# Optimization experiments

Hardware: AMD Instinct MI355X
Metric: run time of the kernel (lower is better)

## Reference

```python
import jax, jax.numpy as jnp
import numpy as np

B, K, D_H = 4096, 64, 512
N_AGENTS = 64  # sigma value == N_AGENTS means 'unassigned'
NEG_INF = -1e9


def setup_inputs() -> dict:
    key = jax.random.key(0)
    k1, k2, k3 = jax.random.split(key, 3)
    h = jax.random.normal(k1, (B, K, D_H), dtype=jnp.float32)
    # per-agent attention keys (init std=0.01 as in the torch module)
    keys = jax.random.normal(k2, (N_AGENTS, D_H), dtype=jnp.float32) * 0.01
    sigma = jax.random.randint(k3, (B, K), 0, N_AGENTS + 1)  # N_AGENTS == unassigned
    return {"h": h, "keys": keys, "sigma": sigma}


def reference(h, keys, sigma):
    # h: (B, K, d_h); keys: (n_agents, d_h); sigma: (B, K) int ids
    n_agents = keys.shape[0]
    valid = sigma < n_agents                      # (B, K) mask; id==n_agents -> unassigned
    idx = jnp.where(valid, sigma, 0)              # safe gather index
    w = keys[idx]                                 # (B, K, d_h) gathered agent keys
    logits = jnp.einsum('bkd,bkd->bk', w, h)      # per-slot dot-product score
    logits = jnp.where(valid, logits, NEG_INF)
    alpha = jax.nn.softmax(logits, axis=1)        # softmax over K slots
    return jnp.einsum('bk,bkd->bd', alpha, h)     # (B, d_h) weighted pooling
```

## Files before the change

### kernel.cpp

```cpp
#include <hip/hip_runtime.h>


constexpr int K  = 64;
constexpr int D  = 512;
constexpr int NA = 64;
#define NEG_INF (-1e9f)

__global__ __launch_bounds__(512)
void bda_kernel(const float* __restrict__ h, const float* __restrict__ keys,
                const int* __restrict__ sigma, float* __restrict__ out) {
    const int b    = blockIdx.x;
    const int tid  = threadIdx.x;
    const int w    = tid >> 6;
    const int lane = tid & 63;

    __shared__ float lg[K];
    __shared__ __align__(16) float obuf[8 * D];

    const float* hb = h + (size_t)b * (K * D);
    float4 h0[8], h1[8];

#pragma unroll
    for (int kk = 0; kk < 8; ++kk) {
        const int k = (w << 3) + kk;
        const float* hrow = hb + k * D + (lane << 3);
        h0[kk] = ((const float4*)hrow)[0];
        h1[kk] = ((const float4*)hrow)[1];

        const int sg = sigma[b * K + k];
        float dacc = NEG_INF;
        if (sg < NA) {
            const float* krow = keys + sg * D + (lane << 3);
            const float4 k0 = ((const float4*)krow)[0];
            const float4 k1 = ((const float4*)krow)[1];
            dacc = h0[kk].x * k0.x + h0[kk].y * k0.y
                 + h0[kk].z * k0.z + h0[kk].w * k0.w
                 + h1[kk].x * k1.x + h1[kk].y * k1.y
                 + h1[kk].z * k1.z + h1[kk].w * k1.w;
#pragma unroll
            for (int off = 32; off > 0; off >>= 1)
                dacc += __shfl_xor(dacc, off, 64);
        }
        if (lane == 0) lg[k] = dacc;
    }
    __syncthreads();

    const float v = lg[lane];
    float m = v;
#pragma unroll
    for (int off = 32; off > 0; off >>= 1)
        m = fmaxf(m, __shfl_xor(m, off, 64));
    float s = __expf(v - m);
#pragma unroll
    for (int off = 32; off > 0; off >>= 1)
        s += __shfl_xor(s, off, 64);
    const float inv_s = 1.0f / s;

    float4 a0 = make_float4(0.f, 0.f, 0.f, 0.f);
    float4 a1 = make_float4(0.f, 0.f, 0.f, 0.f);
#pragma unroll
    for (int kk = 0; kk < 8; ++kk) {
        const int k = (w << 3) + kk;
        const float al = __expf(lg[k] - m) * inv_s;
        a0.x += al * h0[kk].x;  a0.y += al * h0[kk].y;
        a0.z += al * h0[kk].z;  a0.w += al * h0[kk].w;
        a1.x += al * h1[kk].x;  a1.y += al * h1[kk].y;
        a1.z += al * h1[kk].z;  a1.w += al * h1[kk].w;
    }
    float* ob = obuf + w * D + (lane << 3);
    ((float4*)ob)[0] = a0;
    ((float4*)ob)[1] = a1;
    __syncthreads();

    float r = 0.f;
#pragma unroll
    for (int w2 = 0; w2 < 8; ++w2)
        r += obuf[w2 * D + tid];
    out[(size_t)b * D + tid] = r;
}

extern "C" void kernel_launch(void* const* d_in, const int* in_sizes, int n_in,
                              void* d_out, int out_size, void* d_ws, size_t ws_size,
                              hipStream_t stream) {
    const float* h     = (const float*)d_in[0];
    const float* keys  = (const float*)d_in[1];
    const int*   sigma = (const int*)d_in[2];
    float*       out   = (float*)d_out;
    const int B = in_sizes[2] / K;
    bda_kernel<<<dim3(B), dim3(512), 0, stream>>>(h, keys, sigma, out);
}
```

Baseline: 671.4 us.

## Hoist all h loads, vectorize sigma loads, and use transposed butterfly reduction

Issues all 16 float4 loads of h up front, before any reduction, so the memory requests overlap instead of being serialized behind the per-row shuffle reductions. Sigma is now read as two int4 vector loads, and keys are loaded unconditionally with a clamped index so there is no divergent branch. The eight per-row 64-lane reductions are merged into a transposed butterfly that needs fewer shuffles in total. Launch bounds now request 4 blocks per CU, which caps registers and may cause spills given the 64 floats of h held per thread.

```diff
diff --git a/kernel.cpp b/kernel.cpp
--- a/kernel.cpp
+++ b/kernel.cpp
@@ -6,7 +6,7 @@
 constexpr int NA = 64;
 #define NEG_INF (-1e9f)
 
-__global__ __launch_bounds__(512)
+__global__ __launch_bounds__(512, 4)
 void bda_kernel(const float* __restrict__ h, const float* __restrict__ keys,
                 const int* __restrict__ sigma, float* __restrict__ out) {
     const int b    = blockIdx.x;
@@ -18,39 +18,61 @@
     __shared__ __align__(16) float obuf[8 * D];
 
     const float* hb = h + (size_t)b * (K * D);
+
     float4 h0[8], h1[8];
+#pragma unroll
+    for (int kk = 0; kk < 8; ++kk) {
+        const float* hrow = hb + ((w << 3) + kk) * D + (lane << 3);
+        h0[kk] = ((const float4*)hrow)[0];
+        h1[kk] = ((const float4*)hrow)[1];
+    }
+
+    const int4* sp = (const int4*)(sigma + b * K + (w << 3));
+    const int4 sA = sp[0];
+    const int4 sB = sp[1];
+    const int sgarr[8] = {sA.x, sA.y, sA.z, sA.w, sB.x, sB.y, sB.z, sB.w};
+
+    float d[8];
+#pragma unroll
+    for (int kk = 0; kk < 8; ++kk) {
+        const int  sg    = sgarr[kk];
+        const bool valid = (sg < NA);
+        const int  si    = valid ? sg : 0;
+        const float* krow = keys + si * D + (lane << 3);
+        const float4 k0 = ((const float4*)krow)[0];
+        const float4 k1 = ((const float4*)krow)[1];
+        const float acc = h0[kk].x * k0.x + h0[kk].y * k0.y
+                        + h0[kk].z * k0.z + h0[kk].w * k0.w
+                        + h1[kk].x * k1.x + h1[kk].y * k1.y
+                        + h1[kk].z * k1.z + h1[kk].w * k1.w;
+        d[kk] = valid ? acc : NEG_INF;
+    }
 
 #pragma unroll
     for (int kk = 0; kk < 8; ++kk) {
-        const int k = (w << 3) + kk;
-        const float* hrow = hb + k * D + (lane << 3);
-        h0[kk] = ((const float4*)hrow)[0];
-        h1[kk] = ((const float4*)hrow)[1];
-
-        const int sg = sigma[b * K + k];
-        float dacc = NEG_INF;
-        if (sg < NA) {
-            const float* krow = keys + sg * D + (lane << 3);
-            const float4 k0 = ((const float4*)krow)[0];
-            const float4 k1 = ((const float4*)krow)[1];
-            dacc = h0[kk].x * k0.x + h0[kk].y * k0.y
-                 + h0[kk].z * k0.z + h0[kk].w * k0.w
-                 + h1[kk].x * k1.x + h1[kk].y * k1.y
-                 + h1[kk].z * k1.z + h1[kk].w * k1.w;
-#pragma unroll
-            for (int off = 32; off > 0; off >>= 1)
-                dacc += __shfl_xor(dacc, off, 64);
-        }
-        if (lane == 0) lg[k] = dacc;
+        d[kk] += __shfl_xor(d[kk], 1, 64);
+        d[kk] += __shfl_xor(d[kk], 2, 64);
+        d[kk] += __shfl_xor(d[kk], 4, 64);
     }
+    const float s0 = (lane & 1) ? d[1] : d[0];
+    const float s1 = (lane & 1) ? d[3] : d[2];
+    const float s2 = (lane & 1) ? d[5] : d[4];
+    const float s3 = (lane & 1) ? d[7] : d[6];
+    const float t0 = (lane & 2) ? s1 : s0;
+    const float t1 = (lane & 2) ? s3 : s2;
+    float v        = (lane & 4) ? t1 : t0;
+    v += __shfl_xor(v, 8, 64);
+    v += __shfl_xor(v, 16, 64);
+    v += __shfl_xor(v, 32, 64);
+    if (lane < 8) lg[(w << 3) + lane] = v;
     __syncthreads();
 
-    const float v = lg[lane];
-    float m = v;
+    const float vl = lg[lane];
+    float m = vl;
 #pragma unroll
     for (int off = 32; off > 0; off >>= 1)
         m = fmaxf(m, __shfl_xor(m, off, 64));
-    float s = __expf(v - m);
+    float s = __expf(vl - m);
 #pragma unroll
     for (int off = 32; off > 0; off >>= 1)
         s += __shfl_xor(s, off, 64);
@@ -60,8 +82,7 @@
     float4 a1 = make_float4(0.f, 0.f, 0.f, 0.f);
 #pragma unroll
     for (int kk = 0; kk < 8; ++kk) {
-        const int k = (w << 3) + kk;
-        const float al = __expf(lg[k] - m) * inv_s;
+        const float al = __expf(lg[(w << 3) + kk] - m) * inv_s;
         a0.x += al * h0[kk].x;  a0.y += al * h0[kk].y;
         a0.z += al * h0[kk].z;  a0.w += al * h0[kk].w;
         a1.x += al * h1[kk].x;  a1.y += al * h1[kk].y;
```

Result: no change. 678.7 us (+1.1%).
